# Kernel optimization log

Measured on AMD Instinct MI355X. Metric: run time of the kernel, lower is better.

## Reference

```python
import jax, jax.numpy as jnp
import numpy as np

B, C, H, W = 2, 256, 64, 64
HEADS = 8
HEAD_DIM = C // HEADS  # 32
INNER = HEADS * HEAD_DIM  # 256
GROUPS = 32
EPS = 1e-5


def groupnorm(x, w, b):
    # x: [B, C, H, W]; normalize over (C//G, H, W) within each of G groups
    Bx, Cx, Hx, Wx = x.shape
    xg = x.reshape(Bx, GROUPS, -1)
    mu = xg.mean(axis=-1, keepdims=True)
    var = xg.var(axis=-1, keepdims=True)
    xn = ((xg - mu) * jax.lax.rsqrt(var + EPS)).reshape(Bx, Cx, Hx, Wx)
    return xn * w[:, None, None] + b[:, None, None]


def setup_inputs() -> dict:
    key = jax.random.key(0)
    k0, k1, k2 = jax.random.split(key, 3)
    x = jax.random.normal(k0, (B, C, H, W), dtype=jnp.float32)
    gn_weight = jnp.ones((C,), dtype=jnp.float32)
    gn_bias = jnp.zeros((C,), dtype=jnp.float32)
    # 1x1 conv weights (kernel dims squeezed): [out_ch, in_ch]
    w_qkv = jax.random.normal(k1, (3 * INNER, C), dtype=jnp.float32) * 0.02
    w_out = jax.random.normal(k2, (C, INNER), dtype=jnp.float32) * 0.02
    return {"x": x, "gn_weight": gn_weight, "gn_bias": gn_bias,
            "w_qkv": w_qkv, "w_out": w_out}


def reference(x, gn_weight, gn_bias, w_qkv, w_out):
    Bx, Cx, Hx, Wx = x.shape
    N = Hx * Wx
    scale = HEAD_DIM ** -0.5
    xn = groupnorm(x, gn_weight, gn_bias)
    # 1x1 conv == channel matmul
    qkv = jnp.einsum('oc,bchw->bohw', w_qkv, xn)  # [B, 3*INNER, H, W]
    q, k, v = jnp.split(qkv, 3, axis=1)
    # 'b (h d) x y -> b h (x y) d'
    def to_heads(t):
        return t.reshape(Bx, HEADS, HEAD_DIM, N).transpose(0, 1, 3, 2)  # bhnd
    q, k, v = to_heads(q), to_heads(k), to_heads(v)
    sim = jnp.einsum('bhid,bhjd->bhij', q, k) * scale  # [B, h, N, N]
    attn = jax.nn.softmax(sim, axis=-1)
    o = jnp.einsum('bhij,bhjd->bhid', attn, v)  # [B, h, N, d]
    # 'b h (x y) d -> b (h d) x y'
    o = o.transpose(0, 1, 3, 2).reshape(Bx, INNER, Hx, Wx)
    out = jnp.einsum('co,bohw->bchw', w_out, o)
    return x + out
```

## Files before the change

### kernel.cpp

```cpp
#include <hip/hip_runtime.h>
#include <hip/hip_bf16.h>

#define BATCH 2
#define CH 256
#define HW 4096
#define HEADS 8
#define HDIM 32
#define GROUPS 32
#define EPS 1e-5f
#define SCALE 0.17677669529663687f
#define QSCALE (0.17677669529663687f * 1.4426950408889634f)

typedef short s16x8 __attribute__((ext_vector_type(8)));
typedef float floatx4 __attribute__((ext_vector_type(4)));
typedef unsigned short ushort_t;
typedef unsigned int uint_t;

static __device__ __forceinline__ ushort_t f2bf(float f) {
    __hip_bfloat16 h = __float2bfloat16(f);
    return *reinterpret_cast<ushort_t*>(&h);
}

static __device__ __forceinline__ uint_t pk2(float lo, float hi) {
    return __builtin_amdgcn_perm(__float_as_uint(hi), __float_as_uint(lo), 0x07060302u);
}

static __device__ __forceinline__ void gload_lds16(const ushort_t* g, ushort_t* l) {
    __builtin_amdgcn_global_load_lds((const __attribute__((address_space(1))) void*)g,
                                     (__attribute__((address_space(3))) void*)l, 16, 0, 0);
}

__global__ void wcvt(const float* __restrict__ wq, const float* __restrict__ wo,
                     ushort_t* __restrict__ dst) {
    int i = blockIdx.x * 256 + threadIdx.x;
    float4 v = (i < 49152) ? ((const float4*)wq)[i] : ((const float4*)wo)[i - 49152];
    ushort_t p[4] = {f2bf(v.x), f2bf(v.y), f2bf(v.z), f2bf(v.w)};
    uint2 o;
    o.x = (uint_t)p[0] | ((uint_t)p[1] << 16);
    o.y = (uint_t)p[2] | ((uint_t)p[3] << 16);
    *(uint2*)&dst[(size_t)i * 4] = o;
}

__global__ void gn_stats(const float* __restrict__ x, float* __restrict__ stats) {
    int bg = blockIdx.x;
    const float4* xv = (const float4*)(x + (size_t)bg * 8 * HW);
    int t = threadIdx.x;
    float s = 0.f, ss = 0.f;
    for (int i = t; i < 8192; i += 256) {
        float4 v = xv[i];
        s  += v.x + v.y + v.z + v.w;
        ss += v.x*v.x + v.y*v.y + v.z*v.z + v.w*v.w;
    }
    #pragma unroll
    for (int off = 32; off; off >>= 1) {
        s  += __shfl_down(s, off);
        ss += __shfl_down(ss, off);
    }
    __shared__ float rs[4], rss[4];
    int wave = t >> 6;
    if ((t & 63) == 0) { rs[wave] = s; rss[wave] = ss; }
    __syncthreads();
    if (t == 0) {
        s  = rs[0] + rs[1] + rs[2] + rs[3];
        ss = rss[0] + rss[1] + rss[2] + rss[3];
        float mu  = s / 32768.f;
        float var = ss / 32768.f - mu * mu;
        stats[bg * 2]     = mu;
        stats[bg * 2 + 1] = rsqrtf(var + EPS);
    }
}

__global__ void norm_transpose(const float* __restrict__ x, const float* __restrict__ stats,
                               const float* __restrict__ gw, const float* __restrict__ gb,
                               ushort_t* __restrict__ xn) {
    __shared__ ushort_t tile[64][40];
    int b = blockIdx.z, c0 = blockIdx.y * 32, n0 = blockIdx.x * 64;
    int t = threadIdx.x;
    #pragma unroll
    for (int i = 0; i < 8; i++) {
        int idx = i * 256 + t;
        int c = idx >> 6, n = idx & 63;
        int cc = c0 + c;
        float mu   = stats[(b * GROUPS + (cc >> 3)) * 2];
        float rstd = stats[(b * GROUPS + (cc >> 3)) * 2 + 1];
        float v = x[((size_t)b * CH + cc) * HW + n0 + n];
        v = (v - mu) * rstd * gw[cc] + gb[cc];
        tile[n][c] = f2bf(v);
    }
    __syncthreads();
    int n = t >> 2, chk = t & 3;
    uint4 val = *(const uint4*)&tile[n][chk * 8];
    *(uint4*)(xn + ((size_t)(b * HW + n0 + n)) * CH + c0 + chk * 8) = val;
}

__global__ void qkv_gemm(const ushort_t* __restrict__ xn, const ushort_t* __restrict__ wqb,
                         ushort_t* __restrict__ qo, ushort_t* __restrict__ ko,
                         ushort_t* __restrict__ vo) {
    __shared__ ushort_t Al[64][40];
    __shared__ ushort_t Bl[64][40];
    int b = blockIdx.z;
    int n0 = blockIdx.x * 64, o0 = blockIdx.y * 64;
    int t = threadIdx.x, lane = t & 63, wave = t >> 6;
    int lr = lane & 15, lk = lane >> 4;
    floatx4 acc[4] = {};
    for (int k0 = 0; k0 < 256; k0 += 32) {
        int row = t >> 2, chk = t & 3;
        *(uint4*)&Al[row][chk * 8] =
            *(const uint4*)(xn + ((size_t)(b * HW + n0 + row)) * CH + k0 + chk * 8);
        *(uint4*)&Bl[row][chk * 8] =
            *(const uint4*)(wqb + (size_t)(o0 + row) * CH + k0 + chk * 8);
        __syncthreads();
        s16x8 af = *(const s16x8*)&Al[wave * 16 + lr][lk * 8];
        #pragma unroll
        for (int ct = 0; ct < 4; ct++) {
            s16x8 bf = *(const s16x8*)&Bl[ct * 16 + lr][lk * 8];
            acc[ct] = __builtin_amdgcn_mfma_f32_16x16x32_bf16(af, bf, acc[ct], 0, 0, 0);
        }
        __syncthreads();
    }
    #pragma unroll
    for (int ct = 0; ct < 4; ct++) {
        int o = o0 + ct * 16 + lr;
        int sel = o >> 8;
        int h = (o >> 5) & 7;
        int d = o & 31;
        int nrow0 = n0 + wave * 16 + (lk << 2);
        if (sel == 0) {
            #pragma unroll
            for (int r = 0; r < 4; r++)
                qo[(((size_t)(b * HEADS + h)) * HW + nrow0 + r) * HDIM + d] =
                    f2bf(acc[ct][r] * QSCALE);
        } else if (sel == 1) {
            #pragma unroll
            for (int r = 0; r < 4; r++) {
                int tt = (nrow0 + r) & 63;
                int sg = 4 * ((tt >> 3) & 3) + 16 * ((((tt >> 2) & 1) << 1) | ((tt >> 5) & 1)) + (tt & 3);
                ko[(((size_t)(b * HEADS + h)) * HW + n0 + sg) * HDIM + d] = f2bf(acc[ct][r]);
            }
        } else {
            ushort_t pk[4];
            #pragma unroll
            for (int r = 0; r < 4; r++) pk[r] = f2bf(acc[ct][r]);
            *(uint2*)&vo[(((size_t)(b * HEADS + h)) * HDIM + d) * HW + nrow0] = *(uint2*)pk;
        }
    }
}

__global__ void __launch_bounds__(256, 4)
attn7(const ushort_t* __restrict__ qg, const ushort_t* __restrict__ kg,
      const ushort_t* __restrict__ vg, ushort_t* __restrict__ og) {
    __shared__ ushort_t Kl[4][2048];
    __shared__ ushort_t Vl[4][2048];
    const int bh = blockIdx.y;
    const int n0 = blockIdx.x * 64;
    const int t = threadIdx.x;
    const int lane = t & 63, w = t >> 6;
    const int lr = lane & 15, lk = lane >> 4;

    const ushort_t* kb = kg + (size_t)bh * HW * HDIM;
    const ushort_t* vb = vg + (size_t)bh * HDIM * HW;

    const int lrr = t & 15, lkk = (t >> 4) & 3, wv = t >> 6;
    const ushort_t* gk = kb + ((wv << 4) + lrr) * HDIM + lkk * 8;
    const ushort_t* gv = vb + (size_t)(((t >> 7) << 4) + lrr) * HW + ((t >> 6) & 1) * 32 + lkk * 8;
    ushort_t* kd0 = &Kl[0][wv << 9]; ushort_t* kd1 = &Kl[1][wv << 9];
    ushort_t* kd2 = &Kl[2][wv << 9]; ushort_t* kd3 = &Kl[3][wv << 9];
    ushort_t* vd0 = &Vl[0][wv << 9]; ushort_t* vd1 = &Vl[1][wv << 9];
    ushort_t* vd2 = &Vl[2][wv << 9]; ushort_t* vd3 = &Vl[3][wv << 9];

    s16x8 qf = *(const s16x8*)(qg + ((size_t)bh * HW + n0 + w * 16 + lr) * HDIM + lk * 8);
    asm volatile("s_waitcnt vmcnt(0)" ::: "memory");

    const s16x8 onesf = {0x3F80, 0x3F80, 0x3F80, 0x3F80, 0x3F80, 0x3F80, 0x3F80, 0x3F80};
    const floatx4 zf = {};
    floatx4 oacc[2] = {};
    floatx4 Lacc = {};

    auto stage = [&](ushort_t* kdn, ushort_t* vdn) {
        gload_lds16(gk, kdn);
        gload_lds16(gv, vdn);
        gk += 64 * HDIM; gv += 64;
    };
    auto compute = [&](const ushort_t* Kb, const ushort_t* Vb) {
        floatx4 sim[4];
        __builtin_amdgcn_s_setprio(1);
#pragma unroll
        for (int ct = 0; ct < 4; ct++) {
            s16x8 kf = *(const s16x8*)(Kb + ct * 512 + lane * 8);
            sim[ct] = __builtin_amdgcn_mfma_f32_16x16x32_bf16(kf, qf, zf, 0, 0, 0);
        }
        __builtin_amdgcn_s_setprio(0);
        s16x8 vf[4];
#pragma unroll
        for (int i = 0; i < 4; i++)
            vf[i] = *(const s16x8*)(Vb + i * 512 + lane * 8);
        float p[4][4];
#pragma unroll
        for (int ct = 0; ct < 4; ct++)
#pragma unroll
            for (int r = 0; r < 4; r++) p[ct][r] = __builtin_amdgcn_exp2f(sim[ct][r]);
        s16x8 pf[2];
#pragma unroll
        for (int s = 0; s < 2; s++) {
            union { uint_t u[4]; s16x8 v; } pu;
            pu.u[0] = pk2(p[s][0], p[s][1]);
            pu.u[1] = pk2(p[s][2], p[s][3]);
            pu.u[2] = pk2(p[s + 2][0], p[s + 2][1]);
            pu.u[3] = pk2(p[s + 2][2], p[s + 2][3]);
            pf[s] = pu.v;
        }
        __builtin_amdgcn_s_setprio(1);
#pragma unroll
        for (int s = 0; s < 2; s++) {
            oacc[0] = __builtin_amdgcn_mfma_f32_16x16x32_bf16(vf[s],     pf[s], oacc[0], 0, 0, 0);
            oacc[1] = __builtin_amdgcn_mfma_f32_16x16x32_bf16(vf[2 + s], pf[s], oacc[1], 0, 0, 0);
            Lacc    = __builtin_amdgcn_mfma_f32_16x16x32_bf16(onesf,     pf[s], Lacc,    0, 0, 0);
        }
        __builtin_amdgcn_s_setprio(0);
    };

#define WN4 { asm volatile("s_waitcnt vmcnt(4)" ::: "memory"); __builtin_amdgcn_s_barrier(); }
#define WN2 { asm volatile("s_waitcnt vmcnt(2)" ::: "memory"); __builtin_amdgcn_s_barrier(); }
#define WN0 { asm volatile("s_waitcnt vmcnt(0)" ::: "memory"); __builtin_amdgcn_s_barrier(); }

    stage(kd0, vd0);
    stage(kd1, vd1);

    for (int it = 0; it < 15; it++) {
        stage(kd2, vd2); WN4 compute(Kl[0], Vl[0]);
        stage(kd3, vd3); WN4 compute(Kl[1], Vl[1]);
        stage(kd0, vd0); WN4 compute(Kl[2], Vl[2]);
        stage(kd1, vd1); WN4 compute(Kl[3], Vl[3]);
    }
    stage(kd2, vd2); WN4 compute(Kl[0], Vl[0]);
    stage(kd3, vd3); WN4 compute(Kl[1], Vl[1]);
    WN2 compute(Kl[2], Vl[2]);
    WN0 compute(Kl[3], Vl[3]);
#undef WN4
#undef WN2
#undef WN0

    const int b = bh >> 3, h = bh & 7;
    float inv = 1.0f / Lacc[0];
    int n = n0 + w * 16 + lr;
#pragma unroll
    for (int ct2 = 0; ct2 < 2; ct2++) {
        uint_t lo = (uint_t)f2bf(oacc[ct2][0] * inv) | ((uint_t)f2bf(oacc[ct2][1] * inv) << 16);
        uint_t hi = (uint_t)f2bf(oacc[ct2][2] * inv) | ((uint_t)f2bf(oacc[ct2][3] * inv) << 16);
        uint2 val = {lo, hi};
        *(uint2*)(og + ((size_t)b * HW + n) * CH + h * 32 + ct2 * 16 + lk * 4) = val;
    }
}

__global__ void proj_res(const ushort_t* __restrict__ oa, const ushort_t* __restrict__ wob,
                         const float* __restrict__ x, float* __restrict__ out) {
    __shared__ ushort_t Al[64][40];
    __shared__ ushort_t Bl[64][40];
    int m0 = blockIdx.x * 64;
    int c0 = blockIdx.y * 64;
    int t = threadIdx.x, lane = t & 63, wave = t >> 6;
    int lr = lane & 15, lk = lane >> 4;
    floatx4 acc[4] = {};
    for (int k0 = 0; k0 < 256; k0 += 32) {
        int row = t >> 2, chk = t & 3;
        *(uint4*)&Al[row][chk * 8] =
            *(const uint4*)(oa + (size_t)(m0 + row) * CH + k0 + chk * 8);
        *(uint4*)&Bl[row][chk * 8] =
            *(const uint4*)(wob + (size_t)(c0 + row) * CH + k0 + chk * 8);
        __syncthreads();
        s16x8 af = *(const s16x8*)&Al[wave * 16 + lr][lk * 8];
        #pragma unroll
        for (int ct = 0; ct < 4; ct++) {
            s16x8 bf = *(const s16x8*)&Bl[ct * 16 + lr][lk * 8];
            acc[ct] = __builtin_amdgcn_mfma_f32_16x16x32_bf16(af, bf, acc[ct], 0, 0, 0);
        }
        __syncthreads();
    }
    int mrow0 = m0 + wave * 16 + (lk << 2);
    int b = mrow0 >> 12;
    int n = mrow0 & 4095;
    #pragma unroll
    for (int ct = 0; ct < 4; ct++) {
        int c = c0 + ct * 16 + lr;
        const float4 xv = *(const float4*)(x + ((size_t)(b * CH + c)) * HW + n);
        float4 ov;
        ov.x = acc[ct][0] + xv.x;
        ov.y = acc[ct][1] + xv.y;
        ov.z = acc[ct][2] + xv.z;
        ov.w = acc[ct][3] + xv.w;
        *(float4*)(out + ((size_t)(b * CH + c)) * HW + n) = ov;
    }
}

extern "C" void kernel_launch(void* const* d_in, const int* in_sizes, int n_in,
                              void* d_out, int out_size, void* d_ws, size_t ws_size,
                              hipStream_t stream) {
    const float* x    = (const float*)d_in[0];
    const float* gw   = (const float*)d_in[1];
    const float* gb   = (const float*)d_in[2];
    const float* wqkv = (const float*)d_in[3];
    const float* wout = (const float*)d_in[4];
    float* out = (float*)d_out;

    char* ws = (char*)d_ws;
    float* stats = (float*)ws;
    ushort_t* xn = (ushort_t*)(ws + 512);
    size_t per = (size_t)BATCH * HW * CH;
    ushort_t* q   = xn + per;
    ushort_t* k   = q + per;
    ushort_t* v   = k + per;
    ushort_t* oa  = v + per;
    ushort_t* wqb = oa + per;
    ushort_t* wob = wqb + 196608;

    wcvt<<<256, 256, 0, stream>>>(wqkv, wout, wqb);
    gn_stats<<<64, 256, 0, stream>>>(x, stats);
    norm_transpose<<<dim3(64, 8, 2), 256, 0, stream>>>(x, stats, gw, gb, xn);
    qkv_gemm<<<dim3(64, 12, 2), 256, 0, stream>>>(xn, wqb, q, k, v);
    attn7<<<dim3(64, 16), 256, 0, stream>>>(q, k, v, oa);
    proj_res<<<dim3(128, 4), 256, 0, stream>>>(oa, wob, x, out);
}
```

Before: 93.90 us.

## Merge weight-convert into GN stats, register-prefetch GEMMs, restructure attention pipeline

Merges the weight conversion kernel into the group-norm statistics kernel, saving one launch. Both GEMM kernels now prefetch the next K-slice into registers while the current slice is computed. The attention kernel moves from a four-slot ring with partial vmcnt waits to a two-stage double buffer with 128-key chunks and full waits plus __syncthreads. The exp2 calls are also inlined into the packing step. The coarser attention synchronisation could expose load latency that the deeper ring previously hid.

```diff
diff --git a/kernel.cpp b/kernel.cpp
--- a/kernel.cpp
+++ b/kernel.cpp
@@ -30,18 +30,19 @@
                                      (__attribute__((address_space(3))) void*)l, 16, 0, 0);
 }
 
-__global__ void wcvt(const float* __restrict__ wq, const float* __restrict__ wo,
-                     ushort_t* __restrict__ dst) {
-    int i = blockIdx.x * 256 + threadIdx.x;
-    float4 v = (i < 49152) ? ((const float4*)wq)[i] : ((const float4*)wo)[i - 49152];
-    ushort_t p[4] = {f2bf(v.x), f2bf(v.y), f2bf(v.z), f2bf(v.w)};
-    uint2 o;
-    o.x = (uint_t)p[0] | ((uint_t)p[1] << 16);
-    o.y = (uint_t)p[2] | ((uint_t)p[3] << 16);
-    *(uint2*)&dst[(size_t)i * 4] = o;
-}
-
-__global__ void gn_stats(const float* __restrict__ x, float* __restrict__ stats) {
+__global__ void gn_stats_wcvt(const float* __restrict__ x, float* __restrict__ stats,
+                              const float* __restrict__ wq, const float* __restrict__ wo,
+                              ushort_t* __restrict__ wdst) {
+    if (blockIdx.x >= 64) {
+        int i = (blockIdx.x - 64) * 256 + threadIdx.x;
+        float4 v = (i < 49152) ? ((const float4*)wq)[i] : ((const float4*)wo)[i - 49152];
+        ushort_t p[4] = {f2bf(v.x), f2bf(v.y), f2bf(v.z), f2bf(v.w)};
+        uint2 o;
+        o.x = (uint_t)p[0] | ((uint_t)p[1] << 16);
+        o.y = (uint_t)p[2] | ((uint_t)p[3] << 16);
+        *(uint2*)&wdst[(size_t)i * 4] = o;
+        return;
+    }
     int bg = blockIdx.x;
     const float4* xv = (const float4*)(x + (size_t)bg * 8 * HW);
     int t = threadIdx.x;
@@ -102,14 +103,20 @@
     int n0 = blockIdx.x * 64, o0 = blockIdx.y * 64;
     int t = threadIdx.x, lane = t & 63, wave = t >> 6;
     int lr = lane & 15, lk = lane >> 4;
+    int row = t >> 2, chk = t & 3;
+    const ushort_t* asrc = xn + ((size_t)(b * HW + n0 + row)) * CH + chk * 8;
+    const ushort_t* bsrc = wqb + (size_t)(o0 + row) * CH + chk * 8;
     floatx4 acc[4] = {};
-    for (int k0 = 0; k0 < 256; k0 += 32) {
-        int row = t >> 2, chk = t & 3;
-        *(uint4*)&Al[row][chk * 8] =
-            *(const uint4*)(xn + ((size_t)(b * HW + n0 + row)) * CH + k0 + chk * 8);
-        *(uint4*)&Bl[row][chk * 8] =
-            *(const uint4*)(wqb + (size_t)(o0 + row) * CH + k0 + chk * 8);
+    uint4 ra = *(const uint4*)(asrc);
+    uint4 rb = *(const uint4*)(bsrc);
+    for (int k0 = 0; k0 < 8; k0++) {
+        *(uint4*)&Al[row][chk * 8] = ra;
+        *(uint4*)&Bl[row][chk * 8] = rb;
         __syncthreads();
+        if (k0 < 7) {
+            ra = *(const uint4*)(asrc + (k0 + 1) * 32);
+            rb = *(const uint4*)(bsrc + (k0 + 1) * 32);
+        }
         s16x8 af = *(const s16x8*)&Al[wave * 16 + lr][lk * 8];
         #pragma unroll
         for (int ct = 0; ct < 4; ct++) {
@@ -147,10 +154,10 @@
 }
 
 __global__ void __launch_bounds__(256, 4)
-attn7(const ushort_t* __restrict__ qg, const ushort_t* __restrict__ kg,
+attn8(const ushort_t* __restrict__ qg, const ushort_t* __restrict__ kg,
       const ushort_t* __restrict__ vg, ushort_t* __restrict__ og) {
-    __shared__ ushort_t Kl[4][2048];
-    __shared__ ushort_t Vl[4][2048];
+    __shared__ ushort_t Kl[2][2][2048];
+    __shared__ ushort_t Vl[2][2][2048];
     const int bh = blockIdx.y;
     const int n0 = blockIdx.x * 64;
     const int t = threadIdx.x;
@@ -161,27 +168,33 @@
     const ushort_t* vb = vg + (size_t)bh * HDIM * HW;
 
     const int lrr = t & 15, lkk = (t >> 4) & 3, wv = t >> 6;
-    const ushort_t* gk = kb + ((wv << 4) + lrr) * HDIM + lkk * 8;
-    const ushort_t* gv = vb + (size_t)(((t >> 7) << 4) + lrr) * HW + ((t >> 6) & 1) * 32 + lkk * 8;
-    ushort_t* kd0 = &Kl[0][wv << 9]; ushort_t* kd1 = &Kl[1][wv << 9];
-    ushort_t* kd2 = &Kl[2][wv << 9]; ushort_t* kd3 = &Kl[3][wv << 9];
-    ushort_t* vd0 = &Vl[0][wv << 9]; ushort_t* vd1 = &Vl[1][wv << 9];
-    ushort_t* vd2 = &Vl[2][wv << 9]; ushort_t* vd3 = &Vl[3][wv << 9];
+    const ushort_t* gkX = kb + ((wv << 4) + lrr) * HDIM + lkk * 8;
+    const ushort_t* gkY = gkX + 64 * HDIM;
+    const ushort_t* gvX = vb + (size_t)(((t >> 7) << 4) + lrr) * HW + ((t >> 6) & 1) * 32 + lkk * 8;
+    const ushort_t* gvY = gvX + 64;
+    ushort_t* kdX[2] = {&Kl[0][0][wv << 9], &Kl[1][0][wv << 9]};
+    ushort_t* kdY[2] = {&Kl[0][1][wv << 9], &Kl[1][1][wv << 9]};
+    ushort_t* vdX[2] = {&Vl[0][0][wv << 9], &Vl[1][0][wv << 9]};
+    ushort_t* vdY[2] = {&Vl[0][1][wv << 9], &Vl[1][1][wv << 9]};
 
     s16x8 qf = *(const s16x8*)(qg + ((size_t)bh * HW + n0 + w * 16 + lr) * HDIM + lk * 8);
-    asm volatile("s_waitcnt vmcnt(0)" ::: "memory");
 
     const s16x8 onesf = {0x3F80, 0x3F80, 0x3F80, 0x3F80, 0x3F80, 0x3F80, 0x3F80, 0x3F80};
     const floatx4 zf = {};
     floatx4 oacc[2] = {};
     floatx4 Lacc = {};
 
-    auto stage = [&](ushort_t* kdn, ushort_t* vdn) {
-        gload_lds16(gk, kdn);
-        gload_lds16(gv, vdn);
-        gk += 64 * HDIM; gv += 64;
+    auto stage0 = [&]() {
+        gload_lds16(gkX, kdX[0]); gload_lds16(gkY, kdY[0]);
+        gload_lds16(gvX, vdX[0]); gload_lds16(gvY, vdY[0]);
+        gkX += 128 * HDIM; gkY += 128 * HDIM; gvX += 128; gvY += 128;
     };
-    auto compute = [&](const ushort_t* Kb, const ushort_t* Vb) {
+    auto stage1 = [&]() {
+        gload_lds16(gkX, kdX[1]); gload_lds16(gkY, kdY[1]);
+        gload_lds16(gvX, vdX[1]); gload_lds16(gvY, vdY[1]);
+        gkX += 128 * HDIM; gkY += 128 * HDIM; gvX += 128; gvY += 128;
+    };
+    auto computeSub = [&](const ushort_t* Kb, const ushort_t* Vb) {
         floatx4 sim[4];
         __builtin_amdgcn_s_setprio(1);
 #pragma unroll
@@ -194,19 +207,14 @@
 #pragma unroll
         for (int i = 0; i < 4; i++)
             vf[i] = *(const s16x8*)(Vb + i * 512 + lane * 8);
-        float p[4][4];
-#pragma unroll
-        for (int ct = 0; ct < 4; ct++)
-#pragma unroll
-            for (int r = 0; r < 4; r++) p[ct][r] = __builtin_amdgcn_exp2f(sim[ct][r]);
         s16x8 pf[2];
 #pragma unroll
         for (int s = 0; s < 2; s++) {
             union { uint_t u[4]; s16x8 v; } pu;
-            pu.u[0] = pk2(p[s][0], p[s][1]);
-            pu.u[1] = pk2(p[s][2], p[s][3]);
-            pu.u[2] = pk2(p[s + 2][0], p[s + 2][1]);
-            pu.u[3] = pk2(p[s + 2][2], p[s + 2][3]);
+            pu.u[0] = pk2(__builtin_amdgcn_exp2f(sim[s][0]),     __builtin_amdgcn_exp2f(sim[s][1]));
+            pu.u[1] = pk2(__builtin_amdgcn_exp2f(sim[s][2]),     __builtin_amdgcn_exp2f(sim[s][3]));
+            pu.u[2] = pk2(__builtin_amdgcn_exp2f(sim[s + 2][0]), __builtin_amdgcn_exp2f(sim[s + 2][1]));
+            pu.u[3] = pk2(__builtin_amdgcn_exp2f(sim[s + 2][2]), __builtin_amdgcn_exp2f(sim[s + 2][3]));
             pf[s] = pu.v;
         }
         __builtin_amdgcn_s_setprio(1);
@@ -219,26 +227,26 @@
         __builtin_amdgcn_s_setprio(0);
     };
 
-#define WN4 { asm volatile("s_waitcnt vmcnt(4)" ::: "memory"); __builtin_amdgcn_s_barrier(); }
-#define WN2 { asm volatile("s_waitcnt vmcnt(2)" ::: "memory"); __builtin_amdgcn_s_barrier(); }
-#define WN0 { asm volatile("s_waitcnt vmcnt(0)" ::: "memory"); __builtin_amdgcn_s_barrier(); }
-
-    stage(kd0, vd0);
-    stage(kd1, vd1);
-
-    for (int it = 0; it < 15; it++) {
-        stage(kd2, vd2); WN4 compute(Kl[0], Vl[0]);
-        stage(kd3, vd3); WN4 compute(Kl[1], Vl[1]);
-        stage(kd0, vd0); WN4 compute(Kl[2], Vl[2]);
-        stage(kd1, vd1); WN4 compute(Kl[3], Vl[3]);
-    }
-    stage(kd2, vd2); WN4 compute(Kl[0], Vl[0]);
-    stage(kd3, vd3); WN4 compute(Kl[1], Vl[1]);
-    WN2 compute(Kl[2], Vl[2]);
-    WN0 compute(Kl[3], Vl[3]);
-#undef WN4
-#undef WN2
-#undef WN0
+#define SYNCF { asm volatile("s_waitcnt vmcnt(0)" ::: "memory"); __syncthreads(); }
+
+    stage0();
+    SYNCF
+    for (int s2 = 0; s2 < 16; s2++) {
+        stage1();
+        computeSub(&Kl[0][0][0], &Vl[0][0][0]);
+        computeSub(&Kl[0][1][0], &Vl[0][1][0]);
+        SYNCF
+        if (s2 < 15) {
+            stage0();
+            computeSub(&Kl[1][0][0], &Vl[1][0][0]);
+            computeSub(&Kl[1][1][0], &Vl[1][1][0]);
+            SYNCF
+        } else {
+            computeSub(&Kl[1][0][0], &Vl[1][0][0]);
+            computeSub(&Kl[1][1][0], &Vl[1][1][0]);
+        }
+    }
+#undef SYNCF
 
     const int b = bh >> 3, h = bh & 7;
     float inv = 1.0f / Lacc[0];
@@ -260,14 +268,20 @@
     int c0 = blockIdx.y * 64;
     int t = threadIdx.x, lane = t & 63, wave = t >> 6;
     int lr = lane & 15, lk = lane >> 4;
+    int row = t >> 2, chk = t & 3;
+    const ushort_t* asrc = oa + (size_t)(m0 + row) * CH + chk * 8;
+    const ushort_t* bsrc = wob + (size_t)(c0 + row) * CH + chk * 8;
     floatx4 acc[4] = {};
-    for (int k0 = 0; k0 < 256; k0 += 32) {
-        int row = t >> 2, chk = t & 3;
-        *(uint4*)&Al[row][chk * 8] =
-            *(const uint4*)(oa + (size_t)(m0 + row) * CH + k0 + chk * 8);
-        *(uint4*)&Bl[row][chk * 8] =
-            *(const uint4*)(wob + (size_t)(c0 + row) * CH + k0 + chk * 8);
+    uint4 ra = *(const uint4*)(asrc);
+    uint4 rb = *(const uint4*)(bsrc);
+    for (int k0 = 0; k0 < 8; k0++) {
+        *(uint4*)&Al[row][chk * 8] = ra;
+        *(uint4*)&Bl[row][chk * 8] = rb;
         __syncthreads();
+        if (k0 < 7) {
+            ra = *(const uint4*)(asrc + (k0 + 1) * 32);
+            rb = *(const uint4*)(bsrc + (k0 + 1) * 32);
+        }
         s16x8 af = *(const s16x8*)&Al[wave * 16 + lr][lk * 8];
         #pragma unroll
         for (int ct = 0; ct < 4; ct++) {
@@ -313,10 +327,9 @@
     ushort_t* wqb = oa + per;
     ushort_t* wob = wqb + 196608;
 
-    wcvt<<<256, 256, 0, stream>>>(wqkv, wout, wqb);
-    gn_stats<<<64, 256, 0, stream>>>(x, stats);
+    gn_stats_wcvt<<<320, 256, 0, stream>>>(x, stats, wqkv, wout, wqb);
     norm_transpose<<<dim3(64, 8, 2), 256, 0, stream>>>(x, stats, gw, gb, xn);
     qkv_gemm<<<dim3(64, 12, 2), 256, 0, stream>>>(xn, wqb, q, k, v);
-    attn7<<<dim3(64, 16), 256, 0, stream>>>(q, k, v, oa);
+    attn8<<<dim3(64, 16), 256, 0, stream>>>(q, k, v, oa);
     proj_res<<<dim3(128, 4), 256, 0, stream>>>(oa, wob, x, out);
 }
```

Result: faster. 88.28 us (-6.0%).
